# Kernel tuning notes

Measured on AMD Instinct MI355X. Metric: run time of the kernel, lower is better.

The kernel has to match this reference:

```python
import jax, jax.numpy as jnp
import numpy as np

DIM = 256
H = 4
HD = DIM // H
SCALE = HD ** -0.5
W = 10
PAD = W // 2
MAX_LEN = 512


def setup_inputs() -> dict:
    key = jax.random.key(0)
    ks = jax.random.split(key, 32)
    B, T, D = 32, 512, DIM
    def w(k, shape):
        return jax.random.normal(k, shape, dtype=jnp.float32) * 0.02
    inp = {
        'x': jax.random.normal(ks[0], (B, T, D), dtype=jnp.float32),
        # global TemporalAttention params (weights stored as (in,out))
        'gq_w': w(ks[1], (D, D)), 'gq_b': jnp.zeros((D,), jnp.float32),
        'gk_w': w(ks[2], (D, D)), 'gk_b': jnp.zeros((D,), jnp.float32),
        'gv_w': w(ks[3], (D, D)), 'gv_b': jnp.zeros((D,), jnp.float32),
        'go_w': w(ks[4], (D, D)), 'go_b': jnp.zeros((D,), jnp.float32),
        'rel_pos_bias': w(ks[5], (2 * MAX_LEN - 1, H)),
        # local sliding-window attention params
        'lq_w': w(ks[6], (D, D)), 'lq_b': jnp.zeros((D,), jnp.float32),
        'lk_w': w(ks[7], (D, D)), 'lk_b': jnp.zeros((D,), jnp.float32),
        'lv_w': w(ks[8], (D, D)), 'lv_b': jnp.zeros((D,), jnp.float32),
        # pattern attention (only q/k projections matter for returned weights)
        'pattern_embed': jax.random.normal(ks[9], (1, 3, D), dtype=jnp.float32),
        'pq_w': w(ks[10], (D, D)), 'pq_b': jnp.zeros((D,), jnp.float32),
        'pk_w': w(ks[11], (D, D)), 'pk_b': jnp.zeros((D,), jnp.float32),
        # fusion MLP
        'f1_w': w(ks[12], (2 * D, D)), 'f1_b': jnp.zeros((D,), jnp.float32),
        'f2_w': w(ks[13], (D, D)), 'f2_b': jnp.zeros((D,), jnp.float32),
    }
    return inp


def _forward(x, gq_w, gq_b, gk_w, gk_b, gv_w, gv_b, go_w, go_b, rel_pos_bias,
             lq_w, lq_b, lk_w, lk_b, lv_w, lv_b,
             pattern_embed, pq_w, pq_b, pk_w, pk_b,
             f1_w, f1_b, f2_w, f2_b):
    B, T, D = x.shape
    # ---- global temporal attention ----
    q = (x @ gq_w + gq_b).reshape(B, T, H, HD)
    k = (x @ gk_w + gk_b).reshape(B, T, H, HD)
    v = (x @ gv_w + gv_b).reshape(B, T, H, HD)
    attn = jnp.einsum('bthd,bshd->bhts', q, k) * SCALE  # (B,H,T,T)
    pos = jnp.arange(T)
    idx = jnp.clip(pos[None, :] - pos[:, None] + T - 1, 0, 2 * T - 2)  # (T,T)
    attn = attn + jnp.transpose(rel_pos_bias[idx], (2, 0, 1))[None]
    attn_w = jax.nn.softmax(attn, axis=-1)  # dropout = identity in eval
    g_out = jnp.einsum('bhts,bshd->bthd', attn_w, v).reshape(B, T, D)
    global_out = g_out @ go_w + go_b
    # ---- local sliding-window attention (single head over full dim) ----
    x_pad = jnp.pad(x, ((0, 0), (PAD, PAD), (0, 0)))  # zero pad -> k/v get bias
    lq = x @ lq_w + lq_b                      # (B,T,D)
    lk = x_pad @ lk_w + lk_b                  # (B,T+W,D)
    lv = x_pad @ lv_w + lv_b
    widx = jnp.arange(T)[:, None] + jnp.arange(W)[None, :]  # (T,W)
    k_win = lk[:, widx]                       # (B,T,W,D)
    v_win = lv[:, widx]
    l_attn = jax.nn.softmax(jnp.einsum('btd,btwd->btw', lq, k_win) * SCALE, axis=-1)
    local_out = jnp.einsum('btw,btwd->btd', l_attn, v_win)
    # ---- fusion MLP + residual ----
    fused = jnp.concatenate([global_out, local_out], axis=-1)
    output = jax.nn.relu(fused @ f1_w + f1_b) @ f2_w + f2_b + x
    # ---- pattern attention (torch MHA, weights averaged over heads) ----
    pe = jnp.broadcast_to(pattern_embed, (B, 3, D))
    pooled = jnp.mean(x, axis=1, keepdims=True)  # (B,1,D)
    pq = (pooled @ pq_w + pq_b).reshape(B, 1, H, HD)
    pk = (pe @ pk_w + pk_b).reshape(B, 3, H, HD)
    plogits = jnp.einsum('bqhd,bkhd->bhqk', pq, pk) * SCALE  # (B,H,1,3)
    pw = jax.nn.softmax(plogits, axis=-1).mean(axis=1)  # avg over heads -> (B,1,3)
    pattern_scores = pw[:, 0]  # (B,3)
    return output, pattern_scores


def reference(x, gq_w, gq_b, gk_w, gk_b, gv_w, gv_b, go_w, go_b, rel_pos_bias,
              lq_w, lq_b, lk_w, lk_b, lv_w, lv_b,
              pattern_embed, pq_w, pq_b, pk_w, pk_b,
              f1_w, f1_b, f2_w, f2_b):
    return _forward(x, gq_w, gq_b, gk_w, gk_b, gv_w, gv_b, go_w, go_b, rel_pos_bias,
                    lq_w, lq_b, lk_w, lk_b, lv_w, lv_b,
                    pattern_embed, pq_w, pq_b, pk_w, pk_b,
                    f1_w, f1_b, f2_w, f2_b)
```

## Files before the change

### kernel.cpp

```cpp
#include <hip/hip_runtime.h>
#include <hip/hip_bf16.h>

typedef __attribute__((ext_vector_type(8))) __bf16 bf16x8;
typedef __attribute__((ext_vector_type(8))) unsigned short u16x8;
typedef __attribute__((ext_vector_type(4))) float f32x4;

#define MFMA_BF16(a,b,c) __builtin_amdgcn_mfma_f32_16x16x32_bf16((a),(b),(c),0,0,0)

#define ASCALE 0.125f
#define SEQT 512
#define NB 32
#define BT 16384

#define GLD_LDS16(g, l) __builtin_amdgcn_global_load_lds( \
    (__attribute__((address_space(1))) void*)(g), \
    (__attribute__((address_space(3))) void*)(l), 16, 0, 0)

__device__ __forceinline__ unsigned short f2bf(float f) {
    unsigned int u = __float_as_uint(f);
    u += 0x7fffu + ((u >> 16) & 1u);
    return (unsigned short)(u >> 16);
}
__device__ __forceinline__ float bf2f(unsigned short h) {
    return __uint_as_float(((unsigned int)h) << 16);
}

__global__ __launch_bounds__(256) void cast_x_kernel(const float* __restrict__ x,
                                                     unsigned short* __restrict__ xb, int n) {
    int i = (blockIdx.x * 256 + threadIdx.x) * 4;
    if (i < n) {
        float4 v = *(const float4*)(x + i);
        ushort4 o;
        o.x = f2bf(v.x); o.y = f2bf(v.y); o.z = f2bf(v.z); o.w = f2bf(v.w);
        *(ushort4*)(xb + i) = o;
    }
}

__global__ __launch_bounds__(256) void wconv_kernel(const float* __restrict__ src,
                                                    unsigned short* __restrict__ dst, int K) {
    int k = blockIdx.x, n = threadIdx.x;
    dst[(size_t)n * K + k] = f2bf(src[(size_t)k * 256 + n]);
}

__global__ __launch_bounds__(256) void biascat_kernel(const float* b0, const float* b1,
                                                      const float* b2, const float* b3,
                                                      const float* b4, float* out) {
    int j = blockIdx.x, d = threadIdx.x;
    const float* src = (j == 0) ? b0 : (j == 1) ? b1 : (j == 2) ? b2 : (j == 3) ? b3 : b4;
    out[j * 256 + d] = src[d];
}

__global__ __launch_bounds__(256)
void gemm128(const unsigned short* __restrict__ A, const unsigned short* __restrict__ Bt,
             const float* __restrict__ bias, int K,
             void* __restrict__ out, int ldc, int mode, int do_relu, int bias_row,
             const float* __restrict__ resid) {
    __shared__ __align__(16) unsigned short As[128 * 32];
    __shared__ __align__(16) unsigned short Bs[128 * 32];
    const int tid = threadIdx.x;
    const int w = tid >> 6, l = tid & 63, g = l >> 4, rl = l & 15;
    const int wm = w >> 1, wn = w & 1;
    const int m0 = blockIdx.x * 128, n0 = blockIdx.y * 128;
    const int srow = l >> 2, scol = (l & 3) * 8;

    f32x4 acc[4][4];
    #pragma unroll
    for (int m = 0; m < 4; ++m)
        #pragma unroll
        for (int n = 0; n < 4; ++n) acc[m][n] = (f32x4){0.f, 0.f, 0.f, 0.f};

    for (int k0 = 0; k0 < K; k0 += 32) {
        #pragma unroll
        for (int j = 0; j < 2; ++j) {
            int c = w * 2 + j;
            const unsigned short* ga = A  + (size_t)(m0 + c * 16 + srow) * K + k0 + scol;
            const unsigned short* gb = Bt + (size_t)(n0 + c * 16 + srow) * K + k0 + scol;
            GLD_LDS16(ga, As + c * 512);
            GLD_LDS16(gb, Bs + c * 512);
        }
        __syncthreads();
        bf16x8 af[4], bfr[4];
        #pragma unroll
        for (int m = 0; m < 4; ++m) af[m]  = *(const bf16x8*)&As[(wm * 64 + m * 16 + rl) * 32 + g * 8];
        #pragma unroll
        for (int n = 0; n < 4; ++n) bfr[n] = *(const bf16x8*)&Bs[(wn * 64 + n * 16 + rl) * 32 + g * 8];
        #pragma unroll
        for (int m = 0; m < 4; ++m)
            #pragma unroll
            for (int n = 0; n < 4; ++n)
                acc[m][n] = MFMA_BF16(af[m], bfr[n], acc[m][n]);
        __syncthreads();
    }

    const int crow0 = m0 + wm * 64, ccol0 = n0 + wn * 64;
    #pragma unroll
    for (int m = 0; m < 4; ++m) {
        #pragma unroll
        for (int n = 0; n < 4; ++n) {
            #pragma unroll
            for (int r = 0; r < 4; ++r) {
                int row = crow0 + m * 16 + g * 4 + r;
                int col = ccol0 + n * 16 + rl;
                float v = acc[m][n][r] + (bias_row ? bias[row] : bias[col]);
                if (do_relu) v = fmaxf(v, 0.f);
                if (mode == 0) {
                    ((unsigned short*)out)[(size_t)row * ldc + col] = f2bf(v);
                } else {
                    float res = resid ? resid[(size_t)row * ldc + col] : 0.f;
                    ((float*)out)[(size_t)row * ldc + col] = v + res;
                }
            }
        }
    }
}

__global__ __launch_bounds__(256)
void attn_global2(const unsigned short* __restrict__ proj, const unsigned short* __restrict__ vT,
                  const float* __restrict__ rpb, unsigned short* __restrict__ gout) {
    __shared__ __align__(16) unsigned short Ks[64][72];
    __shared__ __align__(16) unsigned short Vs[64][72];
    __shared__ __align__(16) unsigned short Ps[64][72];
    __shared__ float rb_s[127];

    const int tid = threadIdx.x;
    const int w = tid >> 6, l = tid & 63, g = l >> 4, rl = l & 15;
    const int bh = blockIdx.y, b = bh >> 2, h = bh & 3;
    const int t0 = blockIdx.x * 64;

    bf16x8 qf[2];
    #pragma unroll
    for (int kk = 0; kk < 2; ++kk)
        qf[kk] = *(const bf16x8*)(proj + (size_t)(b * SEQT + t0 + w * 16 + rl) * 1280
                                  + h * 64 + kk * 32 + g * 8);

    f32x4 oacc[4];
    #pragma unroll
    for (int n = 0; n < 4; ++n) oacc[n] = (f32x4){0.f, 0.f, 0.f, 0.f};
    float lpart[4] = {0.f, 0.f, 0.f, 0.f};

    for (int s0 = 0; s0 < SEQT; s0 += 64) {
        __syncthreads();
        #pragma unroll
        for (int cc = 0; cc < 2; ++cc) {
            int c = tid + cc * 256;
            int sr = c >> 3, hc = c & 7;
            u16x8 kv = *(const u16x8*)(proj + (size_t)(b * SEQT + s0 + sr) * 1280
                                       + 256 + h * 64 + hc * 8);
            *(u16x8*)&Ks[sr][hc * 8] = kv;
            u16x8 vv = *(const u16x8*)(vT + (size_t)(h * 64 + sr) * BT
                                       + b * SEQT + s0 + hc * 8);
            *(u16x8*)&Vs[sr][hc * 8] = vv;
        }
        if (tid < 127) {
            int dd = s0 - t0 + 448 + tid;
            rb_s[tid] = rpb[dd * 4 + h];
        }
        __syncthreads();

        f32x4 sacc[4];
        #pragma unroll
        for (int n = 0; n < 4; ++n) sacc[n] = (f32x4){0.f, 0.f, 0.f, 0.f};
        #pragma unroll
        for (int kk = 0; kk < 2; ++kk) {
            #pragma unroll
            for (int n = 0; n < 4; ++n) {
                bf16x8 kf = *(const bf16x8*)&Ks[n * 16 + rl][kk * 32 + g * 8];
                sacc[n] = MFMA_BF16(qf[kk], kf, sacc[n]);
            }
        }

        #pragma unroll
        for (int n = 0; n < 4; ++n) {
            #pragma unroll
            for (int r = 0; r < 4; ++r) {
                int relc = (n * 16 + rl) - (w * 16 + g * 4 + r) + 63;
                float p = __expf(sacc[n][r] * ASCALE + rb_s[relc]);
                lpart[r] += p;
                Ps[w * 16 + g * 4 + r][n * 16 + rl] = f2bf(p);
            }
        }

        #pragma unroll
        for (int kk = 0; kk < 2; ++kk) {
            bf16x8 pf = *(const bf16x8*)&Ps[w * 16 + rl][kk * 32 + g * 8];
            #pragma unroll
            for (int n = 0; n < 4; ++n) {
                bf16x8 vf = *(const bf16x8*)&Vs[n * 16 + rl][kk * 32 + g * 8];
                oacc[n] = MFMA_BF16(pf, vf, oacc[n]);
            }
        }
    }

    #pragma unroll
    for (int r = 0; r < 4; ++r) {
        #pragma unroll
        for (int mk = 1; mk < 16; mk <<= 1) lpart[r] += __shfl_xor(lpart[r], mk);
    }
    const size_t obase = (size_t)b * SEQT * 256 + h * 64;
    #pragma unroll
    for (int n = 0; n < 4; ++n) {
        #pragma unroll
        for (int r = 0; r < 4; ++r) {
            float o = oacc[n][r] / lpart[r];
            gout[obase + (size_t)(t0 + w * 16 + g * 4 + r) * 256 + n * 16 + rl] = f2bf(o);
        }
    }
}

__global__ __launch_bounds__(256)
void local_attn(const unsigned short* __restrict__ proj,
                const float* __restrict__ lk_bias, const float* __restrict__ lv_bias,
                unsigned short* __restrict__ fused) {
    const int tid = threadIdx.x;
    const int wv = tid >> 6, lane = tid & 63;
    const int row = blockIdx.x * 4 + wv;
    const int b = row >> 9, tt = row & 511;

    ushort4 qv = *((const ushort4*)(proj + (size_t)row * 1280 + 512) + lane);
    float qf[4] = {bf2f(qv.x), bf2f(qv.y), bf2f(qv.z), bf2f(qv.w)};

    float sw[10];
    #pragma unroll
    for (int w = 0; w < 10; ++w) {
        int src = tt + w - 5;
        float kf[4];
        if (src >= 0 && src < 512) {
            ushort4 kv = *((const ushort4*)(proj + (size_t)(b * 512 + src) * 1280 + 768) + lane);
            kf[0] = bf2f(kv.x); kf[1] = bf2f(kv.y); kf[2] = bf2f(kv.z); kf[3] = bf2f(kv.w);
        } else {
            float4 kb4 = *((const float4*)lk_bias + lane);
            kf[0] = kb4.x; kf[1] = kb4.y; kf[2] = kb4.z; kf[3] = kb4.w;
        }
        float p = qf[0] * kf[0] + qf[1] * kf[1] + qf[2] * kf[2] + qf[3] * kf[3];
        #pragma unroll
        for (int mk = 1; mk < 64; mk <<= 1) p += __shfl_xor(p, mk);
        sw[w] = p * ASCALE;
    }
    float mx = sw[0];
    #pragma unroll
    for (int w = 1; w < 10; ++w) mx = fmaxf(mx, sw[w]);
    float pv[10], s = 0.f;
    #pragma unroll
    for (int w = 0; w < 10; ++w) { pv[w] = __expf(sw[w] - mx); s += pv[w]; }
    float inv = 1.f / s;

    float of[4] = {0.f, 0.f, 0.f, 0.f};
    #pragma unroll
    for (int w = 0; w < 10; ++w) {
        int src = tt + w - 5;
        float vf[4];
        if (src >= 0 && src < 512) {
            ushort4 vv = *((const ushort4*)(proj + (size_t)(b * 512 + src) * 1280 + 1024) + lane);
            vf[0] = bf2f(vv.x); vf[1] = bf2f(vv.y); vf[2] = bf2f(vv.z); vf[3] = bf2f(vv.w);
        } else {
            float4 vb4 = *((const float4*)lv_bias + lane);
            vf[0] = vb4.x; vf[1] = vb4.y; vf[2] = vb4.z; vf[3] = vb4.w;
        }
        float pw = pv[w] * inv;
        of[0] += pw * vf[0]; of[1] += pw * vf[1]; of[2] += pw * vf[2]; of[3] += pw * vf[3];
    }
    ushort4 o;
    o.x = f2bf(of[0]); o.y = f2bf(of[1]); o.z = f2bf(of[2]); o.w = f2bf(of[3]);
    *((ushort4*)(fused + (size_t)row * 512 + 256) + lane) = o;
}

__global__ __launch_bounds__(256)
void pooled_mean2(const float* __restrict__ x, float* __restrict__ pooled) {
    int b = blockIdx.x >> 3, tc = blockIdx.x & 7;
    int d = threadIdx.x;
    const float* xp = x + ((size_t)b * SEQT + tc * 64) * 256 + d;
    float s = 0.f;
    #pragma unroll 8
    for (int t = 0; t < 64; ++t) s += xp[(size_t)t * 256];
    atomicAdd(&pooled[b * 256 + d], s * (1.0f / 512.0f));
}

__global__ __launch_bounds__(256)
void pattern_k(const float* __restrict__ pooled, const float* __restrict__ pe,
               const float* __restrict__ pq_w, const float* __restrict__ pq_b,
               const float* __restrict__ pk_w, const float* __restrict__ pk_b,
               float* __restrict__ out_scores) {
    __shared__ float pool_s[256];
    __shared__ float pes[3 * 256];
    __shared__ float pq_s[256];
    __shared__ float pk_s[3][256];
    __shared__ float pw_s[4][3];
    int b = blockIdx.x, d = threadIdx.x;
    pool_s[d] = pooled[b * 256 + d];
    pes[d] = pe[d]; pes[256 + d] = pe[256 + d]; pes[512 + d] = pe[512 + d];
    __syncthreads();
    float acc = pq_b[d];
    for (int k = 0; k < 256; ++k) acc += pool_s[k] * pq_w[k * 256 + d];
    pq_s[d] = acc;
    for (int j = 0; j < 3; ++j) {
        float a = pk_b[d];
        for (int k = 0; k < 256; ++k) a += pes[j * 256 + k] * pk_w[k * 256 + d];
        pk_s[j][d] = a;
    }
    __syncthreads();
    int h = d >> 6, lane = d & 63;
    float lg[3];
    #pragma unroll
    for (int j = 0; j < 3; ++j) {
        float p = pq_s[h * 64 + lane] * pk_s[j][h * 64 + lane];
        #pragma unroll
        for (int mk = 1; mk < 64; mk <<= 1) p += __shfl_xor(p, mk);
        lg[j] = p * ASCALE;
    }
    float mx = fmaxf(fmaxf(lg[0], lg[1]), lg[2]);
    float e0 = __expf(lg[0] - mx), e1 = __expf(lg[1] - mx), e2 = __expf(lg[2] - mx);
    float sinv = 1.f / (e0 + e1 + e2);
    if (lane == 0) { pw_s[h][0] = e0 * sinv; pw_s[h][1] = e1 * sinv; pw_s[h][2] = e2 * sinv; }
    __syncthreads();
    if (d < 3)
        out_scores[b * 3 + d] = 0.25f * (pw_s[0][d] + pw_s[1][d] + pw_s[2][d] + pw_s[3][d]);
}

extern "C" void kernel_launch(void* const* d_in, const int* in_sizes, int n_in,
                              void* d_out, int out_size, void* d_ws, size_t ws_size,
                              hipStream_t stream) {
    (void)in_sizes; (void)n_in; (void)out_size; (void)ws_size;
    const float* x    = (const float*)d_in[0];
    const float* gq_w = (const float*)d_in[1];  const float* gq_b = (const float*)d_in[2];
    const float* gk_w = (const float*)d_in[3];  const float* gk_b = (const float*)d_in[4];
    const float* gv_w = (const float*)d_in[5];  const float* gv_b = (const float*)d_in[6];
    const float* go_w = (const float*)d_in[7];  const float* go_b = (const float*)d_in[8];
    const float* rpb  = (const float*)d_in[9];
    const float* lq_w = (const float*)d_in[10]; const float* lq_b = (const float*)d_in[11];
    const float* lk_w = (const float*)d_in[12]; const float* lk_b = (const float*)d_in[13];
    const float* lv_w = (const float*)d_in[14]; const float* lv_b = (const float*)d_in[15];
    const float* pe   = (const float*)d_in[16];
    const float* pq_w = (const float*)d_in[17]; const float* pq_b = (const float*)d_in[18];
    const float* pk_w = (const float*)d_in[19]; const float* pk_b = (const float*)d_in[20];
    const float* f1_w = (const float*)d_in[21]; const float* f1_b = (const float*)d_in[22];
    const float* f2_w = (const float*)d_in[23]; const float* f2_b = (const float*)d_in[24];

    char* ws = (char*)d_ws;
    const size_t MB = 1024 * 1024;
    unsigned short* xb    = (unsigned short*)(ws + 0);
    unsigned short* proj  = (unsigned short*)(ws + 8 * MB);
    unsigned short* vT    = (unsigned short*)(ws + 48 * MB);
    unsigned short* fused = (unsigned short*)(ws + 56 * MB);
    unsigned short* hb    = (unsigned short*)(ws + 72 * MB);
    unsigned short* wts   = (unsigned short*)(ws + 80 * MB);
    unsigned short* gv_t  = wts;
    unsigned short* go_t  = gv_t + 65536;
    unsigned short* f1_t  = go_t + 65536;
    unsigned short* f2_t  = f1_t + 131072;
    unsigned short* wcat  = f2_t + 65536;
    float* bcat   = (float*)(ws + 82 * MB);
    float* pooled = (float*)(ws + 83 * MB);

    float* out = (float*)d_out;
    float* out_scores = out + (size_t)BT * 256;

    cast_x_kernel<<<4096, 256, 0, stream>>>(x, xb, BT * 256);
    wconv_kernel<<<256, 256, 0, stream>>>(gq_w, wcat + 0 * 65536, 256);
    wconv_kernel<<<256, 256, 0, stream>>>(gk_w, wcat + 1 * 65536, 256);
    wconv_kernel<<<256, 256, 0, stream>>>(lq_w, wcat + 2 * 65536, 256);
    wconv_kernel<<<256, 256, 0, stream>>>(lk_w, wcat + 3 * 65536, 256);
    wconv_kernel<<<256, 256, 0, stream>>>(lv_w, wcat + 4 * 65536, 256);
    wconv_kernel<<<256, 256, 0, stream>>>(gv_w, gv_t, 256);
    wconv_kernel<<<256, 256, 0, stream>>>(go_w, go_t, 256);
    wconv_kernel<<<512, 256, 0, stream>>>(f1_w, f1_t, 512);
    wconv_kernel<<<256, 256, 0, stream>>>(f2_w, f2_t, 256);
    biascat_kernel<<<5, 256, 0, stream>>>(gq_b, gk_b, lq_b, lk_b, lv_b, bcat);

    gemm128<<<dim3(BT / 128, 10), 256, 0, stream>>>(xb, wcat, bcat, 256, proj, 1280, 0, 0, 0, nullptr);
    gemm128<<<dim3(2, BT / 128), 256, 0, stream>>>(gv_t, xb, gv_b, 256, vT, BT, 0, 0, 1, nullptr);

    attn_global2<<<dim3(SEQT / 64, NB * 4), 256, 0, stream>>>(proj, vT, rpb, xb);

    gemm128<<<dim3(BT / 128, 2), 256, 0, stream>>>(xb, go_t, go_b, 256, fused, 512, 0, 0, 0, nullptr);

    local_attn<<<BT / 4, 256, 0, stream>>>(proj, lk_b, lv_b, fused);

    gemm128<<<dim3(BT / 128, 2), 256, 0, stream>>>(fused, f1_t, f1_b, 512, hb, 256, 0, 1, 0, nullptr);
    gemm128<<<dim3(BT / 128, 2), 256, 0, stream>>>(hb, f2_t, f2_b, 256, out, 256, 1, 0, 0, x);

    hipMemsetAsync(pooled, 0, 32 * 256 * sizeof(float), stream);
    pooled_mean2<<<256, 256, 0, stream>>>(x, pooled);
    pattern_k<<<NB, 256, 0, stream>>>(pooled, pe, pq_w, pq_b, pk_w, pk_b, out_scores);
}
```

Before: 355.5 us.

## Double-buffer GEMM, add 64-wide tiles, batch weight conversion, drop pooled atomics

Replaces the GEMM with a double-buffered variant that prefetches the next K slice into LDS while computing the current one. A BN=64 tile variant is added and used for the narrow GEMMs to launch more blocks. The nine weight-transpose launches and the bias concat merge into one tiled LDS-transpose kernel. The pooled mean now reads bf16 x into partial buffers that pattern_k sums, which removes the memset and the atomics but adds bf16 rounding error to pattern scores.

```diff
diff --git a/kernel.cpp b/kernel.cpp
--- a/kernel.cpp
+++ b/kernel.cpp
@@ -36,71 +36,109 @@
     }
 }
 
-__global__ __launch_bounds__(256) void wconv_kernel(const float* __restrict__ src,
-                                                    unsigned short* __restrict__ dst, int K) {
-    int k = blockIdx.x, n = threadIdx.x;
-    dst[(size_t)n * K + k] = f2bf(src[(size_t)k * 256 + n]);
-}
-
-__global__ __launch_bounds__(256) void biascat_kernel(const float* b0, const float* b1,
-                                                      const float* b2, const float* b3,
-                                                      const float* b4, float* out) {
-    int j = blockIdx.x, d = threadIdx.x;
-    const float* src = (j == 0) ? b0 : (j == 1) ? b1 : (j == 2) ? b2 : (j == 3) ? b3 : b4;
-    out[j * 256 + d] = src[d];
-}
-
+struct WPack {
+    const float* src[9];
+    unsigned short* dst[9];
+    int K[9];
+    const float* bsrc[5];
+    float* bdst;
+};
+
+__global__ __launch_bounds__(256) void wconv_all(WPack p) {
+    const int z = blockIdx.z;
+    const int tid = threadIdx.x;
+    if (z == 9) {
+        int idx = blockIdx.y * 8 + blockIdx.x;
+        if (idx < 5) p.bdst[idx * 256 + tid] = p.bsrc[idx][tid];
+        return;
+    }
+    const int K = p.K[z];
+    const int k0 = blockIdx.x * 64;
+    if (k0 >= K) return;
+    const int n0 = blockIdx.y * 64;
+    __shared__ float tile[64][65];
+    const int tx = tid & 63, ty = tid >> 6;
+    const float* src = p.src[z];
+    #pragma unroll
+    for (int i = 0; i < 16; ++i) {
+        int r = ty * 16 + i;
+        tile[r][tx] = src[(size_t)(k0 + r) * 256 + n0 + tx];
+    }
+    __syncthreads();
+    unsigned short* dst = p.dst[z];
+    #pragma unroll
+    for (int i = 0; i < 16; ++i) {
+        int r = ty * 16 + i;
+        dst[(size_t)(n0 + r) * K + k0 + tx] = f2bf(tile[tx][r]);
+    }
+}
+
+template<int BN>
 __global__ __launch_bounds__(256)
-void gemm128(const unsigned short* __restrict__ A, const unsigned short* __restrict__ Bt,
+void gemm_db(const unsigned short* __restrict__ A, const unsigned short* __restrict__ Bt,
              const float* __restrict__ bias, int K,
              void* __restrict__ out, int ldc, int mode, int do_relu, int bias_row,
              const float* __restrict__ resid) {
-    __shared__ __align__(16) unsigned short As[128 * 32];
-    __shared__ __align__(16) unsigned short Bs[128 * 32];
+    constexpr int BM = 128;
+    constexpr int MF = (BN == 128) ? 4 : 2;
+    constexpr int AR = (BM * 32) / 2048;
+    constexpr int BR = (BN * 32) / 2048;
+    __shared__ __align__(16) unsigned short As[2][BM * 32];
+    __shared__ __align__(16) unsigned short Bs[2][BN * 32];
     const int tid = threadIdx.x;
     const int w = tid >> 6, l = tid & 63, g = l >> 4, rl = l & 15;
-    const int wm = w >> 1, wn = w & 1;
-    const int m0 = blockIdx.x * 128, n0 = blockIdx.y * 128;
-    const int srow = l >> 2, scol = (l & 3) * 8;
-
-    f32x4 acc[4][4];
-    #pragma unroll
-    for (int m = 0; m < 4; ++m)
+    const int wrow = (BN == 128) ? (w >> 1) * 64 : w * 32;
+    const int wcol = (BN == 128) ? (w & 1) * 64 : 0;
+    const int m0 = blockIdx.x * BM, n0 = blockIdx.y * BN;
+
+    f32x4 acc[MF][4];
+    #pragma unroll
+    for (int m = 0; m < MF; ++m)
         #pragma unroll
         for (int n = 0; n < 4; ++n) acc[m][n] = (f32x4){0.f, 0.f, 0.f, 0.f};
 
-    for (int k0 = 0; k0 < K; k0 += 32) {
-        #pragma unroll
-        for (int j = 0; j < 2; ++j) {
-            int c = w * 2 + j;
-            const unsigned short* ga = A  + (size_t)(m0 + c * 16 + srow) * K + k0 + scol;
-            const unsigned short* gb = Bt + (size_t)(n0 + c * 16 + srow) * K + k0 + scol;
-            GLD_LDS16(ga, As + c * 512);
-            GLD_LDS16(gb, Bs + c * 512);
-        }
-        __syncthreads();
-        bf16x8 af[4], bfr[4];
-        #pragma unroll
-        for (int m = 0; m < 4; ++m) af[m]  = *(const bf16x8*)&As[(wm * 64 + m * 16 + rl) * 32 + g * 8];
-        #pragma unroll
-        for (int n = 0; n < 4; ++n) bfr[n] = *(const bf16x8*)&Bs[(wn * 64 + n * 16 + rl) * 32 + g * 8];
-        #pragma unroll
-        for (int m = 0; m < 4; ++m)
+    auto stage = [&](int buf, int k0) {
+        #pragma unroll
+        for (int j = 0; j < AR; ++j) {
+            int e = j * 256 + tid;
+            GLD_LDS16(A + (size_t)(m0 + (e >> 2)) * K + k0 + (e & 3) * 8, &As[buf][e * 8]);
+        }
+        #pragma unroll
+        for (int j = 0; j < BR; ++j) {
+            int e = j * 256 + tid;
+            GLD_LDS16(Bt + (size_t)(n0 + (e >> 2)) * K + k0 + (e & 3) * 8, &Bs[buf][e * 8]);
+        }
+    };
+
+    const int NIT = K >> 5;
+    stage(0, 0);
+    __syncthreads();
+    for (int it = 0; it < NIT; ++it) {
+        const int cur = it & 1;
+        if (it + 1 < NIT) stage(cur ^ 1, (it + 1) * 32);
+        bf16x8 af[MF], bfr[4];
+        #pragma unroll
+        for (int m = 0; m < MF; ++m)
+            af[m] = *(const bf16x8*)&As[cur][(wrow + m * 16 + rl) * 32 + g * 8];
+        #pragma unroll
+        for (int n = 0; n < 4; ++n)
+            bfr[n] = *(const bf16x8*)&Bs[cur][(wcol + n * 16 + rl) * 32 + g * 8];
+        #pragma unroll
+        for (int m = 0; m < MF; ++m)
             #pragma unroll
             for (int n = 0; n < 4; ++n)
                 acc[m][n] = MFMA_BF16(af[m], bfr[n], acc[m][n]);
         __syncthreads();
     }
 
-    const int crow0 = m0 + wm * 64, ccol0 = n0 + wn * 64;
-    #pragma unroll
-    for (int m = 0; m < 4; ++m) {
+    #pragma unroll
+    for (int m = 0; m < MF; ++m) {
         #pragma unroll
         for (int n = 0; n < 4; ++n) {
             #pragma unroll
             for (int r = 0; r < 4; ++r) {
-                int row = crow0 + m * 16 + g * 4 + r;
-                int col = ccol0 + n * 16 + rl;
+                int row = m0 + wrow + m * 16 + g * 4 + r;
+                int col = n0 + wcol + n * 16 + rl;
                 float v = acc[m][n][r] + (bias_row ? bias[row] : bias[col]);
                 if (do_relu) v = fmaxf(v, 0.f);
                 if (mode == 0) {
@@ -265,18 +303,18 @@
 }
 
 __global__ __launch_bounds__(256)
-void pooled_mean2(const float* __restrict__ x, float* __restrict__ pooled) {
+void pooled_part(const unsigned short* __restrict__ xb, float* __restrict__ pp) {
     int b = blockIdx.x >> 3, tc = blockIdx.x & 7;
     int d = threadIdx.x;
-    const float* xp = x + ((size_t)b * SEQT + tc * 64) * 256 + d;
+    const unsigned short* xp = xb + ((size_t)b * SEQT + tc * 64) * 256 + d;
     float s = 0.f;
     #pragma unroll 8
-    for (int t = 0; t < 64; ++t) s += xp[(size_t)t * 256];
-    atomicAdd(&pooled[b * 256 + d], s * (1.0f / 512.0f));
+    for (int t = 0; t < 64; ++t) s += bf2f(xp[(size_t)t * 256]);
+    pp[(size_t)(tc * 32 + b) * 256 + d] = s * (1.0f / 512.0f);
 }
 
 __global__ __launch_bounds__(256)
-void pattern_k(const float* __restrict__ pooled, const float* __restrict__ pe,
+void pattern_k(const float* __restrict__ pp, const float* __restrict__ pe,
                const float* __restrict__ pq_w, const float* __restrict__ pq_b,
                const float* __restrict__ pk_w, const float* __restrict__ pk_b,
                float* __restrict__ out_scores) {
@@ -286,7 +324,10 @@
     __shared__ float pk_s[3][256];
     __shared__ float pw_s[4][3];
     int b = blockIdx.x, d = threadIdx.x;
-    pool_s[d] = pooled[b * 256 + d];
+    float ps = 0.f;
+    #pragma unroll
+    for (int tc = 0; tc < 8; ++tc) ps += pp[(size_t)(tc * 32 + b) * 256 + d];
+    pool_s[d] = ps;
     pes[d] = pe[d]; pes[256 + d] = pe[256 + d]; pes[512 + d] = pe[512 + d];
     __syncthreads();
     float acc = pq_b[d];
@@ -348,37 +389,39 @@
     unsigned short* f1_t  = go_t + 65536;
     unsigned short* f2_t  = f1_t + 131072;
     unsigned short* wcat  = f2_t + 65536;
-    float* bcat   = (float*)(ws + 82 * MB);
-    float* pooled = (float*)(ws + 83 * MB);
+    float* bcat = (float*)(ws + 82 * MB);
+    float* pp   = (float*)(ws + 83 * MB);
 
     float* out = (float*)d_out;
     float* out_scores = out + (size_t)BT * 256;
 
     cast_x_kernel<<<4096, 256, 0, stream>>>(x, xb, BT * 256);
-    wconv_kernel<<<256, 256, 0, stream>>>(gq_w, wcat + 0 * 65536, 256);
-    wconv_kernel<<<256, 256, 0, stream>>>(gk_w, wcat + 1 * 65536, 256);
-    wconv_kernel<<<256, 256, 0, stream>>>(lq_w, wcat + 2 * 65536, 256);
-    wconv_kernel<<<256, 256, 0, stream>>>(lk_w, wcat + 3 * 65536, 256);
-    wconv_kernel<<<256, 256, 0, stream>>>(lv_w, wcat + 4 * 65536, 256);
-    wconv_kernel<<<256, 256, 0, stream>>>(gv_w, gv_t, 256);
-    wconv_kernel<<<256, 256, 0, stream>>>(go_w, go_t, 256);
-    wconv_kernel<<<512, 256, 0, stream>>>(f1_w, f1_t, 512);
-    wconv_kernel<<<256, 256, 0, stream>>>(f2_w, f2_t, 256);
-    biascat_kernel<<<5, 256, 0, stream>>>(gq_b, gk_b, lq_b, lk_b, lv_b, bcat);
-
-    gemm128<<<dim3(BT / 128, 10), 256, 0, stream>>>(xb, wcat, bcat, 256, proj, 1280, 0, 0, 0, nullptr);
-    gemm128<<<dim3(2, BT / 128), 256, 0, stream>>>(gv_t, xb, gv_b, 256, vT, BT, 0, 0, 1, nullptr);
+    WPack p;
+    p.src[0] = gq_w; p.dst[0] = wcat + 0 * 65536; p.K[0] = 256;
+    p.src[1] = gk_w; p.dst[1] = wcat + 1 * 65536; p.K[1] = 256;
+    p.src[2] = lq_w; p.dst[2] = wcat + 2 * 65536; p.K[2] = 256;
+    p.src[3] = lk_w; p.dst[3] = wcat + 3 * 65536; p.K[3] = 256;
+    p.src[4] = lv_w; p.dst[4] = wcat + 4 * 65536; p.K[4] = 256;
+    p.src[5] = gv_w; p.dst[5] = gv_t;  p.K[5] = 256;
+    p.src[6] = go_w; p.dst[6] = go_t;  p.K[6] = 256;
+    p.src[7] = f1_w; p.dst[7] = f1_t;  p.K[7] = 512;
+    p.src[8] = f2_w; p.dst[8] = f2_t;  p.K[8] = 256;
+    p.bsrc[0] = gq_b; p.bsrc[1] = gk_b; p.bsrc[2] = lq_b; p.bsrc[3] = lk_b; p.bsrc[4] = lv_b;
+    p.bdst = bcat;
+    wconv_all<<<dim3(8, 4, 10), 256, 0, stream>>>(p);
+    pooled_part<<<256, 256, 0, stream>>>(xb, pp);
+
+    gemm_db<128><<<dim3(BT / 128, 10), 256, 0, stream>>>(xb, wcat, bcat, 256, proj, 1280, 0, 0, 0, nullptr);
+    gemm_db<64><<<dim3(2, BT / 64), 256, 0, stream>>>(gv_t, xb, gv_b, 256, vT, BT, 0, 0, 1, nullptr);
 
     attn_global2<<<dim3(SEQT / 64, NB * 4), 256, 0, stream>>>(proj, vT, rpb, xb);
 
-    gemm128<<<dim3(BT / 128, 2), 256, 0, stream>>>(xb, go_t, go_b, 256, fused, 512, 0, 0, 0, nullptr);
+    gemm_db<64><<<dim3(BT / 128, 4), 256, 0, stream>>>(xb, go_t, go_b, 256, fused, 512, 0, 0, 0, nullptr);
 
     local_attn<<<BT / 4, 256, 0, stream>>>(proj, lk_b, lv_b, fused);
 
-    gemm128<<<dim3(BT / 128, 2), 256, 0, stream>>>(fused, f1_t, f1_b, 512, hb, 256, 0, 1, 0, nullptr);
-    gemm128<<<dim3(BT / 128, 2), 256, 0, stream>>>(hb, f2_t, f2_b, 256, out, 256, 1, 0, 0, x);
-
-    hipMemsetAsync(pooled, 0, 32 * 256 * sizeof(float), stream);
-    pooled_mean2<<<256, 256, 0, stream>>>(x, pooled);
-    pattern_k<<<NB, 256, 0, stream>>>(pooled, pe, pq_w, pq_b, pk_w, pk_b, out_scores);
-}
+    gemm_db<64><<<dim3(BT / 128, 4), 256, 0, stream>>>(fused, f1_t, f1_b, 512, hb, 256, 0, 1, 0, nullptr);
+    gemm_db<64><<<dim3(BT / 128, 4), 256, 0, stream>>>(hb, f2_t, f2_b, 256, out, 256, 1, 0, 0, x);
+
+    pattern_k<<<NB, 256, 0, stream>>>(pp, pe, pq_w, pq_b, pk_w, pk_b, out_scores);
+}
```

Result: faster. 299.7 us (-15.7%).
